# Optimization experiments

Measured on AMD Instinct MI355X. Metric: run time of the kernel, lower is better.

Reference implementation:

```python
import jax, jax.numpy as jnp
import numpy as np

N, H, B = 4096, 128, 32
K_MSG, K_INT = 32, 20
CUTOFFS = (3.0, 3.0, 6.0, 6.0, 10.0, 10.0)  # two EGNN layers per backbone
silu = jax.nn.silu


def _lin(key, fi, fo):
    s = 1.0 / np.sqrt(fi)
    return jax.random.uniform(key, (fi, fo), jnp.float32, -s, s)


def setup_inputs():
    ks = jax.random.split(jax.random.key(0), 16)
    L = 6

    def stack(k, fi, fo):
        return jnp.stack([_lin(kk, fi, fo) for kk in jax.random.split(k, L)])

    return dict(
        h=jax.random.normal(ks[0], (N, H), jnp.float32),
        pos=3.0 * jax.random.normal(ks[1], (N, 3), jnp.float32),
        batch=jnp.sort(jax.random.randint(ks[2], (N,), 0, B)),
        edge_w1=stack(ks[3], 2 * H + 1, H), edge_b1=jnp.zeros((L, H)),
        edge_w2=stack(ks[4], H, H), edge_b2=jnp.zeros((L, H)),
        coord_w1=stack(ks[5], H, H), coord_b1=jnp.zeros((L, H)),
        coord_w2=stack(ks[6], H, 1),
        node_w1=stack(ks[7], 2 * H, H), node_b1=jnp.zeros((L, H)),
        node_w2=stack(ks[8], H, H), node_b2=jnp.zeros((L, H)),
        fw1=_lin(ks[9], H, 128), fb1=jnp.zeros((128,)),
        fw2=_lin(ks[10], 128, 3), fb2=jnp.zeros((3,)),
        iw=jnp.stack([_lin(kk, 2 * H + 2, 1) for kk in jax.random.split(ks[11], 3)]),
        ib=jnp.zeros((3, 1)),
        cw1=_lin(ks[12], H, 128), cb1=jnp.zeros((128,)),
        cw2=_lin(ks[13], 128, 64), cb2=jnp.zeros((64,)),
        sw=_lin(ks[14], H, 1), sb=jnp.zeros((1,)),
    )


def _neighbors(pos, batch, cutoff, k):
    # radius graph with fixed fan-out: k nearest same-graph neighbors within cutoff
    p = jax.lax.stop_gradient(pos)
    d2 = jnp.sum((p[:, None, :] - p[None, :, :]) ** 2, -1)  # [N,N]
    valid = (batch[:, None] == batch[None, :]) & (~jnp.eye(p.shape[0], dtype=bool)) & (d2 <= cutoff * cutoff)
    neg, idx = jax.lax.top_k(jnp.where(valid, -d2, -jnp.inf), k)
    return idx, neg > -jnp.inf  # [N,k] int, [N,k] bool validity mask


def _egnn_layer(h, pos, idx, mask, ew1, eb1, ew2, eb2, cw1, cb1, cw2, nw1, nb1, nw2, nb2):
    mf = mask[..., None].astype(h.dtype)  # [N,K,1]
    hj = h[idx]                            # [N,K,H] gather
    rel = pos[:, None, :] - pos[idx]       # [N,K,3]
    d2 = jnp.sum(rel * rel, -1, keepdims=True)
    hi = jnp.broadcast_to(h[:, None, :], hj.shape)
    m = silu(jnp.concatenate([hi, hj, d2], -1) @ ew1 + eb1)
    m = silu(m @ ew2 + eb2) * mf           # masked messages [N,K,H]
    c = silu(m @ cw1 + cb1) @ cw2          # per-edge coord weight [N,K,1]
    cnt = jnp.maximum(jnp.sum(mf, 1), 1.0)
    pos = pos + jnp.sum(rel * c * mf, 1) / cnt
    h = h + (silu(jnp.concatenate([h, jnp.sum(m, 1)], -1) @ nw1 + nb1) @ nw2 + nb2)
    return h, pos


def _forward(h, pos, batch, edge_w1, edge_b1, edge_w2, edge_b2, coord_w1, coord_b1, coord_w2,
             node_w1, node_b1, node_w2, node_b2, fw1, fb1, fw2, fb2, iw, ib, cw1, cb1, cw2, cb2, sw, sb):
    idx = mask = None
    for l in range(6):  # short(3.0) x2, medium(6.0) x2, long(10.0) x2
        if l % 2 == 0:
            idx, mask = _neighbors(pos, batch, CUTOFFS[l], K_MSG)
        h, pos = _egnn_layer(h, pos, idx, mask, edge_w1[l], edge_b1[l], edge_w2[l], edge_b2[l],
                             coord_w1[l], coord_b1[l], coord_w2[l],
                             node_w1[l], node_b1[l], node_w2[l], node_b2[l])
    forces = jnp.tanh(h @ fw1 + fb1) @ fw2 + fb2
    # interaction detection: radius graph (r=10, max 20 neighbors)
    iidx, imask = _neighbors(pos, batch, 10.0, K_INT)
    rel = pos[:, None, :] - pos[iidx]
    dist = jnp.sqrt(jnp.sum(rel * rel, -1, keepdims=True) + 1e-12)  # [N,K,1]
    hi = jnp.broadcast_to(h[:, None, :], (h.shape[0], K_INT, h.shape[1]))
    feats = jnp.concatenate([hi, h[iidx], dist, dist / 10.0], -1)  # [N,K,2H+2]
    scores = jax.nn.sigmoid(jnp.einsum('nkf,tfo->tnko', feats, iw) + ib[:, None, None, :])
    scores = scores * imask[None, :, :, None].astype(h.dtype)  # zero padded edges
    conformer = jax.nn.relu(h @ cw1 + cb1) @ cw2 + cb2
    steric = h @ sw + sb
    return h, pos, forces, scores[0], scores[1], scores[2], conformer, steric


def reference(h, pos, batch, edge_w1, edge_b1, edge_w2, edge_b2, coord_w1, coord_b1, coord_w2,
              node_w1, node_b1, node_w2, node_b2, fw1, fb1, fw2, fb2, iw, ib, cw1, cb1, cw2, cb2, sw, sb):
    return _forward(h, pos, batch, edge_w1, edge_b1, edge_w2, edge_b2, coord_w1, coord_b1, coord_w2,
                    node_w1, node_b1, node_w2, node_b2, fw1, fb1, fw2, fb2, iw, ib, cw1, cb1, cw2, cb2, sw, sb)
```

## Files before the change

kernel.cpp:

```cpp
#include <hip/hip_runtime.h>
#include <hip/hip_bf16.h>

#define NN 4096
#define HD 128
#define KE 32
#define KI 20
#define XLD 132
#define PLOF 68

#define OFF_H   0
#define OFF_POS 524288
#define OFF_F   536576
#define OFF_S   548864
#define OFF_C   794624
#define OFF_ST  1056768

typedef unsigned short u16;
typedef unsigned int u32;
typedef unsigned long long u64;
typedef __attribute__((ext_vector_type(8))) short bf16x8;
typedef __attribute__((ext_vector_type(4))) float f32x4;

#define PERM_HI 0x07060302u
#define PERM_LO 0x05040100u

__device__ __forceinline__ float b2f(u16 u) {
  union { u32 i; float f; } c; c.i = ((u32)u) << 16; return c.f;
}
__device__ __forceinline__ float silu_f(float x) { return x / (1.f + __expf(-x)); }
__device__ __forceinline__ void stout(void* out, int fp32m, size_t i, float v) {
  if (fp32m) ((float*)out)[i] = v;
  else ((__hip_bfloat16*)out)[i] = __float2bfloat16(v);
}
__device__ __forceinline__ u32 f2b(float f) {
  u32 u = __float_as_uint(f);
  return (u + 0x7fffu + ((u >> 16) & 1u)) >> 16;
}
__device__ __forceinline__ void packhl2(float a, float b, u32& pa, u32& pb) {
  u32 H, L;
  asm("v_cvt_pk_bf16_f32 %0, %1, %2" : "=v"(H) : "v"(a), "v"(b));
  float hfa = __uint_as_float(H << 16);
  float hfb = __uint_as_float(H & 0xffff0000u);
  asm("v_cvt_pk_bf16_f32 %0, %1, %2" : "=v"(L) : "v"(a - hfa), "v"(b - hfb));
  pa = __builtin_amdgcn_perm(H, L, PERM_LO);
  pb = __builtin_amdgcn_perm(H, L, PERM_HI);
}
__device__ __forceinline__ void packplane(float a, float b, u32& H, u32& L) {
  asm("v_cvt_pk_bf16_f32 %0, %1, %2" : "=v"(H) : "v"(a), "v"(b));
  float hfa = __uint_as_float(H << 16);
  float hfb = __uint_as_float(H & 0xffff0000u);
  asm("v_cvt_pk_bf16_f32 %0, %1, %2" : "=v"(L) : "v"(a - hfa), "v"(b - hfb));
}
__device__ __forceinline__ bf16x8 mk8(u32 a, u32 b, u32 c, u32 d) {
  union { u32 u[4]; bf16x8 v; } t;
  t.u[0] = a; t.u[1] = b; t.u[2] = c; t.u[3] = d; return t.v;
}

__global__ void probe_dtype(const u16* __restrict__ h, int* __restrict__ flag) {
  if (threadIdx.x == 0) atomicExch(flag, 0);
  __syncthreads();
  int bad = 0;
  for (int i = threadIdx.x; i < 8192; i += 256) {
    float v = b2f(h[i]);
    if (!(v > -1000.f && v < 1000.f)) bad = 1;
  }
  if (bad) atomicOr(flag, 1);
}

struct CvtTable {
  const void* src[25];
  int dstoff[25];
  int cnt[25];
};

__global__ void convert_all(CvtTable tab, float* __restrict__ wsf, const int* __restrict__ flag) {
  const int seg = blockIdx.y;
  const int i = blockIdx.x * 256 + threadIdx.x;
  if (i >= tab.cnt[seg]) return;
  float v;
  if (*flag) v = ((const float*)tab.src[seg])[i];
  else       v = b2f(((const u16*)tab.src[seg])[i]);
  wsf[tab.dstoff[seg] + i] = v;
}

__global__ void pack_weights(const float* __restrict__ wsf, int offEW1, int offEW2, int offCW1,
                             u16* __restrict__ WBP) {
  int tid = blockIdx.x * 256 + threadIdx.x;
  if (tid >= 18 * 32768) return;
  int m = tid >> 15;
  int rix = tid & 32767;
  int layer = m / 3, s = m % 3;
  const float* src;
  if (s == 0)      src = wsf + offEW1 + (size_t)layer * 257 * HD + 128 * HD;
  else if (s == 1) src = wsf + offEW2 + (size_t)layer * HD * HD;
  else             src = wsf + offCW1 + (size_t)layer * HD * HD;
  int jh = rix & 15, lane = (rix >> 4) & 63, ot = (rix >> 10) & 7, kt = rix >> 13;
  int j = jh & 7;
  int f = kt * 32 + (lane >> 4) * 8 + j;
  int o = ot * 16 + (lane & 15);
  float v = src[f * HD + o];
  u32 hb = f2b(v);
  float hf = __uint_as_float(hb << 16);
  u32 lb = f2b(v - hf);
  WBP[tid] = (jh < 8) ? (u16)hb : (u16)lb;
}

__global__ void graph_bounds(const int* __restrict__ batch, int* __restrict__ gstart) {
  int n = blockIdx.x * 256 + threadIdx.x;
  if (n >= NN) return;
  int v = batch[n];
  int pv = (n == 0) ? -1 : batch[n - 1];
  for (int b = pv + 1; b <= v; b++) gstart[b] = n;
  if (n == NN - 1) for (int b = v + 1; b <= 32; b++) gstart[b] = NN;
}

__global__ __launch_bounds__(256) void neigh_kernel(
    const float* __restrict__ pos, const int* __restrict__ batch,
    const int* __restrict__ gstart, int* __restrict__ idx, int* __restrict__ cnt,
    int Ksel, float cut2) {
  const int lane = threadIdx.x & 63;
  const int i = blockIdx.x * 4 + (threadIdx.x >> 6);
  const int b = batch[i];
  const int gs = gstart[b];
  const int ge = gstart[b + 1];
  const int span = ge - gs;
  const float px = pos[i * 3 + 0], py = pos[i * 3 + 1], pz = pos[i * 3 + 2];
  u64 key[16];
#pragma unroll
  for (int tq = 0; tq < 16; tq++) {
    u64 k64 = ~0ull;
    if (tq * 64 < span) {
      int j = gs + tq * 64 + lane;
      if (j < ge && j != i) {
        float dx = px - pos[j * 3 + 0];
        float dy = py - pos[j * 3 + 1];
        float dz = pz - pos[j * 3 + 2];
        float d2 = dx * dx + dy * dy + dz * dz;
        if (d2 <= cut2) k64 = (((u64)__float_as_uint(d2)) << 32) | (u32)j;
      }
    }
    key[tq] = k64;
  }
  u64 thresh = 0;
  int myidx = i;
  int mycnt = 0;
  for (int s = 0; s < Ksel; s++) {
    u64 m = ~0ull;
#pragma unroll
    for (int tq = 0; tq < 16; tq++) {
      if (tq * 64 < span) {
        u64 kk = key[tq];
        if (kk >= thresh && kk < m) m = kk;
      }
    }
    for (int off = 32; off > 0; off >>= 1) {
      u64 o = __shfl_down(m, (unsigned)off, 64);
      if (o < m) m = o;
    }
    m = __shfl(m, 0, 64);
    if (m != ~0ull) {
      if (lane == s) myidx = (int)(m & 0xffffffffu);
      mycnt++;
      thresh = m + 1;
    } else break;
  }
  if (lane < Ksel) idx[i * Ksel + lane] = myidx;
  if (lane == 0) cnt[i] = mycnt;
}

__device__ __forceinline__ void mfma_stageP(const u32* xp_, const u16* __restrict__ WP,
                                            int w, int lane, f32x4 acc[4]) {
  const int l16 = lane & 15, q = lane >> 4;
  f32x4 z = {0.f, 0.f, 0.f, 0.f};
  acc[0] = z; acc[1] = z; acc[2] = z; acc[3] = z;
#pragma unroll
  for (int kt = 0; kt < 4; kt++) {
    const u16* wb = WP + (size_t)(((kt * 8 + w) * 64 + lane)) * 16;
    bf16x8 wh = *(const bf16x8*)(wb);
    bf16x8 wl = *(const bf16x8*)(wb + 8);
#pragma unroll
    for (int Et = 0; Et < 4; Et++) {
      const u32* xr = xp_ + (Et * 16 + l16) * XLD + kt * 16 + q * 4;
      bf16x8 ah = *(const bf16x8*)(xr);
      bf16x8 al = *(const bf16x8*)(xr + PLOF);
      acc[Et] = __builtin_amdgcn_mfma_f32_16x16x32_bf16(al, wh, acc[Et], 0, 0, 0);
      acc[Et] = __builtin_amdgcn_mfma_f32_16x16x32_bf16(ah, wl, acc[Et], 0, 0, 0);
      acc[Et] = __builtin_amdgcn_mfma_f32_16x16x32_bf16(ah, wh, acc[Et], 0, 0, 0);
    }
  }
}

__device__ __forceinline__ void mfma_stageI(const u32* xp_, const u16* __restrict__ WP,
                                            int w, int lane, f32x4 acc[4]) {
  const int l16 = lane & 15, q = lane >> 4;
  f32x4 z = {0.f, 0.f, 0.f, 0.f};
  acc[0] = z; acc[1] = z; acc[2] = z; acc[3] = z;
#pragma unroll
  for (int kt = 0; kt < 4; kt++) {
    const u16* wb = WP + (size_t)(((kt * 8 + w) * 64 + lane)) * 16;
    bf16x8 wh = *(const bf16x8*)(wb);
    bf16x8 wl = *(const bf16x8*)(wb + 8);
#pragma unroll
    for (int Et = 0; Et < 4; Et++) {
      const u32* xr = xp_ + (Et * 16 + l16) * XLD + kt * 32 + q * 8;
      uint4 xa = *(const uint4*)(xr);
      uint4 xb = *(const uint4*)(xr + 4);
      bf16x8 ah = mk8(__builtin_amdgcn_perm(xa.y, xa.x, PERM_HI),
                      __builtin_amdgcn_perm(xa.w, xa.z, PERM_HI),
                      __builtin_amdgcn_perm(xb.y, xb.x, PERM_HI),
                      __builtin_amdgcn_perm(xb.w, xb.z, PERM_HI));
      bf16x8 al = mk8(__builtin_amdgcn_perm(xa.y, xa.x, PERM_LO),
                      __builtin_amdgcn_perm(xa.w, xa.z, PERM_LO),
                      __builtin_amdgcn_perm(xb.y, xb.x, PERM_LO),
                      __builtin_amdgcn_perm(xb.w, xb.z, PERM_LO));
      acc[Et] = __builtin_amdgcn_mfma_f32_16x16x32_bf16(al, wh, acc[Et], 0, 0, 0);
      acc[Et] = __builtin_amdgcn_mfma_f32_16x16x32_bf16(ah, wl, acc[Et], 0, 0, 0);
      acc[Et] = __builtin_amdgcn_mfma_f32_16x16x32_bf16(ah, wh, acc[Et], 0, 0, 0);
    }
  }
}

__global__ __launch_bounds__(512, 4) void egnn_layer(
    const float* __restrict__ h_in, const float* __restrict__ pos_in,
    float* __restrict__ h_out, float* __restrict__ pos_out,
    const int* __restrict__ idx, const int* __restrict__ cnt,
    const float* __restrict__ ew1, const float* __restrict__ eb1,
    const float* __restrict__ eb2,
    const float* __restrict__ cb1, const float* __restrict__ cw2,
    const float* __restrict__ nw1, const float* __restrict__ nb1,
    const float* __restrict__ nw2, const float* __restrict__ nb2,
    const u16* __restrict__ wbp) {
  __shared__ __align__(16) u32 xp[64 * XLD];
  __shared__ float hi_s[2][HD], hpart_s[2][HD], msum_s[2][HD], u_s[2][HD];
  __shared__ float red_s[512];
  __shared__ float ce_red[64][8];
  __shared__ float rel_s[3][64], d2_s[64], mf_s[64], ce_s[64];
  __shared__ int idx_s[64], cn_s[2];

  const int t = threadIdx.x;
  const int i0 = blockIdx.x * 2;
  const int e = t & 63;
  const int lane = t & 63;
  const int w = __builtin_amdgcn_readfirstlane(t >> 6);
  const int l16 = lane & 15, q = lane >> 4;
  const int o = w * 16 + l16;

  if (t < 64) idx_s[t] = idx[(size_t)(i0 + (t >> 5)) * KE + (t & 31)];
  else if (t < 66) cn_s[t - 64] = cnt[i0 + (t - 64)];
  if (t >= 256) {
    const int nt = t - 256;
    hi_s[nt >> 7][nt & 127] = h_in[(size_t)(i0 + (nt >> 7)) * HD + (nt & 127)];
  }
  __syncthreads();

  if (t < 64) {
    const int nd = t >> 5, ic = i0 + nd;
    const int j = idx_s[t];
    const float rx = pos_in[ic * 3 + 0] - pos_in[j * 3 + 0];
    const float ry = pos_in[ic * 3 + 1] - pos_in[j * 3 + 1];
    const float rz = pos_in[ic * 3 + 2] - pos_in[j * 3 + 2];
    rel_s[0][t] = rx; rel_s[1][t] = ry; rel_s[2][t] = rz;
    d2_s[t] = rx * rx + ry * ry + rz * rz;
    mf_s[t] = ((t & 31) < cn_s[nd]) ? 1.0f : 0.0f;
  }
  {
    const int j = idx_s[e];
    const int f0 = (t >> 6) * 16;
    const float4* src = (const float4*)(h_in + (size_t)j * HD + f0);
    u32* dh = xp + e * XLD + (f0 >> 1);
#pragma unroll
    for (int qq = 0; qq < 4; qq++) {
      float4 v = src[qq];
      u32 H0, L0, H1, L1;
      packplane(v.x, v.y, H0, L0);
      packplane(v.z, v.w, H1, L1);
      uint2 hh; hh.x = H0; hh.y = H1;
      uint2 ll; ll.x = L0; ll.y = L1;
      *(uint2*)(dh + qq * 2) = hh;
      *(uint2*)(dh + PLOF + qq * 2) = ll;
    }
  }
  {
    const int oo = t & 127, nd = (t >> 7) & 1, hf = t >> 8;
    const float* hsrc = hi_s[nd];
    float hp = 0.f;
#pragma unroll
    for (int f4 = hf * 16; f4 < hf * 16 + 16; f4++) {
      float4 xv = *(const float4*)(hsrc + f4 * 4);
      hp = fmaf(xv.x, ew1[(f4 * 4 + 0) * HD + oo], hp);
      hp = fmaf(xv.y, ew1[(f4 * 4 + 1) * HD + oo], hp);
      hp = fmaf(xv.z, ew1[(f4 * 4 + 2) * HD + oo], hp);
      hp = fmaf(xv.w, ew1[(f4 * 4 + 3) * HD + oo], hp);
    }
    red_s[t] = hp;
  }
  __syncthreads();
  if (t < 256) hpart_s[t >> 7][t & 127] = red_s[t] + red_s[t + 256] + eb1[t & 127];
  __syncthreads();

  {
    f32x4 acc[4];
    mfma_stageP(xp, wbp, w, lane, acc);
    __syncthreads();
    const float w2 = ew1[256 * HD + o];
#pragma unroll
    for (int Et = 0; Et < 4; Et++) {
      const float hp = hpart_s[Et >> 1][o];
      const int e0 = Et * 16 + q * 4;
      float s0 = silu_f(acc[Et][0] + hp + d2_s[e0 + 0] * w2);
      float s1 = silu_f(acc[Et][1] + hp + d2_s[e0 + 1] * w2);
      float s2 = silu_f(acc[Et][2] + hp + d2_s[e0 + 2] * w2);
      float s3 = silu_f(acc[Et][3] + hp + d2_s[e0 + 3] * w2);
      u32 p0, p1, p2, p3;
      packhl2(s0, s1, p0, p1);
      packhl2(s2, s3, p2, p3);
      u32* dst = xp + e0 * XLD + o;
      dst[0] = p0; dst[XLD] = p1; dst[2 * XLD] = p2; dst[3 * XLD] = p3;
    }
  }
  __syncthreads();

  {
    f32x4 acc[4];
    mfma_stageI(xp, wbp + 32768, w, lane, acc);
    __syncthreads();
    const float bb = eb2[o];
    float ms0 = 0.f, ms1 = 0.f;
#pragma unroll
    for (int Et = 0; Et < 4; Et++) {
      const int e0 = Et * 16 + q * 4;
      float mm0 = (mf_s[e0 + 0] != 0.f) ? silu_f(acc[Et][0] + bb) : 0.f;
      float mm1 = (mf_s[e0 + 1] != 0.f) ? silu_f(acc[Et][1] + bb) : 0.f;
      float mm2 = (mf_s[e0 + 2] != 0.f) ? silu_f(acc[Et][2] + bb) : 0.f;
      float mm3 = (mf_s[e0 + 3] != 0.f) ? silu_f(acc[Et][3] + bb) : 0.f;
      if (Et < 2) { ms0 += mm0; ms0 += mm1; ms0 += mm2; ms0 += mm3; }
      else        { ms1 += mm0; ms1 += mm1; ms1 += mm2; ms1 += mm3; }
      u32 p0, p1, p2, p3;
      packhl2(mm0, mm1, p0, p1);
      packhl2(mm2, mm3, p2, p3);
      u32* dst = xp + e0 * XLD + o;
      dst[0] = p0; dst[XLD] = p1; dst[2 * XLD] = p2; dst[3 * XLD] = p3;
    }
    ms0 += __shfl_xor(ms0, 16); ms0 += __shfl_xor(ms0, 32);
    ms1 += __shfl_xor(ms1, 16); ms1 += __shfl_xor(ms1, 32);
    if (lane < 16) {
      msum_s[0][w * 16 + lane] = ms0;
      msum_s[1][w * 16 + lane] = ms1;
    }
  }
  __syncthreads();

  {
    f32x4 acc[4];
    mfma_stageI(xp, wbp + 65536, w, lane, acc);
    const float b1 = cb1[o], c2 = cw2[o];
#pragma unroll
    for (int Et = 0; Et < 4; Et++) {
      const int e0 = Et * 16 + q * 4;
#pragma unroll
      for (int r = 0; r < 4; r++) {
        float p = silu_f(acc[Et][r] + b1) * c2;
        p += __shfl_xor(p, 1);
        p += __shfl_xor(p, 2);
        p += __shfl_xor(p, 4);
        p += __shfl_xor(p, 8);
        if (l16 == 0) ce_red[e0 + r][w] = p;
      }
    }
  }
  __syncthreads();
  if (t < 64) {
    float c = 0.f;
#pragma unroll
    for (int wv = 0; wv < 8; wv++) c += ce_red[t][wv];
    ce_s[t] = (mf_s[t] != 0.f) ? c : 0.f;
  }
  __syncthreads();
  if (t < 6) {
    const int nd = t / 3, ax = t - nd * 3, ic = i0 + nd;
    float s = 0.f;
#pragma unroll
    for (int k = 0; k < 32; k++) s = fmaf(rel_s[ax][nd * 32 + k], ce_s[nd * 32 + k], s);
    const float cntf = fmaxf((float)cn_s[nd], 1.f);
    pos_out[ic * 3 + ax] = pos_in[ic * 3 + ax] + s / cntf;
  }
  {
    const int oo = t & 127, nd = (t >> 7) & 1, ph = t >> 8;
    const float* src = ph ? msum_s[nd] : hi_s[nd];
    const float* Wp = nw1 + (size_t)ph * 128 * HD + oo;
    float p = 0.f;
#pragma unroll
    for (int f4 = 0; f4 < 32; f4++) {
      float4 xv = *(const float4*)(src + f4 * 4);
      p = fmaf(xv.x, Wp[(f4 * 4 + 0) * HD], p);
      p = fmaf(xv.y, Wp[(f4 * 4 + 1) * HD], p);
      p = fmaf(xv.z, Wp[(f4 * 4 + 2) * HD], p);
      p = fmaf(xv.w, Wp[(f4 * 4 + 3) * HD], p);
    }
    red_s[t] = p;
  }
  __syncthreads();
  if (t < 256) u_s[t >> 7][t & 127] = silu_f(red_s[t] + red_s[t + 256] + nb1[t & 127]);
  __syncthreads();
  {
    const int oo = t & 127, nd = (t >> 7) & 1, ph = t >> 8;
    const float* src = u_s[nd] + ph * 64;
    const float* Wp = nw2 + (size_t)ph * 64 * HD + oo;
    float p = 0.f;
#pragma unroll
    for (int f4 = 0; f4 < 16; f4++) {
      float4 xv = *(const float4*)(src + f4 * 4);
      p = fmaf(xv.x, Wp[(f4 * 4 + 0) * HD], p);
      p = fmaf(xv.y, Wp[(f4 * 4 + 1) * HD], p);
      p = fmaf(xv.z, Wp[(f4 * 4 + 2) * HD], p);
      p = fmaf(xv.w, Wp[(f4 * 4 + 3) * HD], p);
    }
    red_s[t] = p;
  }
  __syncthreads();
  if (t < 256) {
    const int nd = t >> 7, oo = t & 127;
    h_out[(size_t)(i0 + nd) * HD + oo] = hi_s[nd][oo] + red_s[t] + red_s[t + 256] + nb2[oo];
  }
}

__global__ __launch_bounds__(256) void heads_kernel(
    const float* __restrict__ h, const float* __restrict__ pos,
    const float* __restrict__ fw1, const float* __restrict__ fb1,
    const float* __restrict__ fw2, const float* __restrict__ fb2,
    const float* __restrict__ cw1g, const float* __restrict__ cb1g,
    const float* __restrict__ cw2g, const float* __restrict__ cb2g,
    const float* __restrict__ sw, const float* __restrict__ sb,
    const float* __restrict__ iw,
    float* __restrict__ At, float* __restrict__ Bt,
    void* __restrict__ out, const int* __restrict__ flag) {
  __shared__ float hi_s[HD], v1[HD], red_s[256];
  const int i = blockIdx.x, t = threadIdx.x;
  const int fm = *flag;
  if (t < HD) hi_s[t] = h[(size_t)i * HD + t];
  __syncthreads();
  const int o = t & 127, ph = t >> 7;
  {
    float p = 0.f;
#pragma unroll 4
    for (int f = ph * 64; f < ph * 64 + 64; f++) p = fmaf(hi_s[f], fw1[f * HD + o], p);
    red_s[t] = p;
  }
  __syncthreads();
  if (t < HD) v1[t] = tanhf(red_s[t] + red_s[t + 128] + fb1[t]);
  __syncthreads();
  if (t < 3) {
    float p = 0.f;
    for (int f = 0; f < HD; f++) p = fmaf(v1[f], fw2[f * 3 + t], p);
    stout(out, fm, OFF_F + (size_t)i * 3 + t, p + fb2[t]);
  }
  __syncthreads();
  {
    float p = 0.f;
#pragma unroll 4
    for (int f = ph * 64; f < ph * 64 + 64; f++) p = fmaf(hi_s[f], cw1g[f * HD + o], p);
    red_s[t] = p;
  }
  __syncthreads();
  if (t < HD) v1[t] = fmaxf(red_s[t] + red_s[t + 128] + cb1g[t], 0.f);
  __syncthreads();
  {
    const int oo = t & 63, pc = t >> 6;
    float p = 0.f;
#pragma unroll 4
    for (int f = pc * 32; f < pc * 32 + 32; f++) p = fmaf(v1[f], cw2g[f * 64 + oo], p);
    red_s[t] = p;
  }
  __syncthreads();
  if (t < 64)
    stout(out, fm, OFF_C + (size_t)i * 64 + t,
          red_s[t] + red_s[t + 64] + red_s[t + 128] + red_s[t + 192] + cb2g[t]);
  __syncthreads();
  if (t < HD) red_s[t] = hi_s[t] * sw[t];
  __syncthreads();
  if (t == 0) {
    float p = 0.f;
    for (int f = 0; f < HD; f++) p += red_s[f];
    stout(out, fm, OFF_ST + (size_t)i, p + sb[0]);
  }
  __syncthreads();
  {
    const int g = t >> 5, l = t & 31;
    float p = 0.f;
    if (g < 6) {
      const int tt = g >> 1, half = g & 1;
#pragma unroll
      for (int r2 = 0; r2 < 4; r2++)
        p = fmaf(hi_s[l * 4 + r2], iw[tt * 258 + half * 128 + l * 4 + r2], p);
    }
    red_s[t] = p;
  }
  __syncthreads();
  if (t < 6) {
    float p = 0.f;
    for (int l = 0; l < 32; l++) p += red_s[t * 32 + l];
    const int tt = t >> 1;
    if ((t & 1) == 0) At[tt * NN + i] = p;
    else Bt[tt * NN + i] = p;
  }
  if (t < HD) stout(out, fm, OFF_H + (size_t)i * HD + t, hi_s[t]);
  if (t >= 128 && t < 131) stout(out, fm, OFF_POS + (size_t)i * 3 + (t - 128), pos[i * 3 + (t - 128)]);
}

__global__ void scores_kernel(const float* __restrict__ pos, const int* __restrict__ idx2,
                              const int* __restrict__ cnt2, const float* __restrict__ At,
                              const float* __restrict__ Bt, const float* __restrict__ iw,
                              const float* __restrict__ ib, void* __restrict__ out,
                              const int* __restrict__ flag) {
  int tid = blockIdx.x * 256 + threadIdx.x;
  if (tid >= 3 * NN * KI) return;
  const int fm = *flag;
  const int tt = tid / (NN * KI);
  const int r = tid % (NN * KI);
  const int n = r / KI;
  const int k = r % KI;
  float v = 0.f;
  if (k < cnt2[n]) {
    int j = idx2[n * KI + k];
    float dx = pos[n * 3 + 0] - pos[j * 3 + 0];
    float dy = pos[n * 3 + 1] - pos[j * 3 + 1];
    float dz = pos[n * 3 + 2] - pos[j * 3 + 2];
    float d2 = dx * dx + dy * dy + dz * dz;
    float dist = sqrtf(d2 + 1e-12f);
    float s = At[tt * NN + n] + Bt[tt * NN + j] + dist * iw[tt * 258 + 256] +
              (dist * 0.1f) * iw[tt * 258 + 257] + ib[tt];
    v = 1.f / (1.f + __expf(-s));
  }
  stout(out, fm, OFF_S + (size_t)tid, v);
}

extern "C" void kernel_launch(void* const* d_in, const int* in_sizes, int n_in,
                              void* d_out, int out_size, void* d_ws, size_t ws_size,
                              hipStream_t stream) {
  (void)in_sizes; (void)n_in; (void)out_size; (void)ws_size;

  float* wsf = (float*)d_ws;
  float* h_a = wsf + 0;
  float* pos_a = wsf + 524288;
  float* h_b = wsf + 536576;
  float* pos_b = wsf + 1060864;
  float* At = wsf + 1073152;
  float* Bt = wsf + 1085440;
  const int W0 = 1097728;

  static const int wcnt[23] = {197376, 768, 98304, 768, 98304, 768, 768,
                               196608, 768, 98304, 768, 16384, 128, 384, 3,
                               774, 3, 16384, 128, 8192, 64, 128, 1};
  int woff[23];
  {
    int o = W0;
    for (int k = 0; k < 23; k++) { woff[k] = o; o += wcnt[k]; }
  }
  const int IOFF = woff[22] + wcnt[22];
  int* ibase = (int*)d_ws;
  int* idx1 = ibase + IOFF;
  int* cnt1 = idx1 + NN * KE;
  int* idx2 = cnt1 + NN;
  int* cnt2 = idx2 + NN * KI;
  int* gstart = cnt2 + NN;
  int* flag = gstart + 33;
  int wboff = (int)((flag + 1) - ibase);
  wboff = (wboff + 3) & ~3;
  u16* WBP = (u16*)(ibase + wboff);

  const float* EW1 = wsf + woff[0];
  const float* EB1 = wsf + woff[1];
  const float* EB2 = wsf + woff[3];
  const float* CB1 = wsf + woff[5];
  const float* CW2 = wsf + woff[6];
  const float* NW1 = wsf + woff[7];
  const float* NB1 = wsf + woff[8];
  const float* NW2 = wsf + woff[9];
  const float* NB2 = wsf + woff[10];
  const float* FW1 = wsf + woff[11];
  const float* FB1 = wsf + woff[12];
  const float* FW2 = wsf + woff[13];
  const float* FB2 = wsf + woff[14];
  const float* IW = wsf + woff[15];
  const float* IB = wsf + woff[16];
  const float* CW1G = wsf + woff[17];
  const float* CB1G = wsf + woff[18];
  const float* CW2G = wsf + woff[19];
  const float* CB2G = wsf + woff[20];
  const float* SW = wsf + woff[21];
  const float* SB = wsf + woff[22];

  probe_dtype<<<1, 256, 0, stream>>>((const u16*)d_in[0], flag);

  CvtTable tab;
  tab.src[0] = d_in[0]; tab.dstoff[0] = 0;       tab.cnt[0] = NN * HD;
  tab.src[1] = d_in[1]; tab.dstoff[1] = 524288;  tab.cnt[1] = NN * 3;
  for (int k = 0; k < 23; k++) {
    tab.src[2 + k] = d_in[3 + k];
    tab.dstoff[2 + k] = woff[k];
    tab.cnt[2 + k] = wcnt[k];
  }
  {
    dim3 g((NN * HD + 255) / 256, 25, 1);
    convert_all<<<g, 256, 0, stream>>>(tab, wsf, flag);
  }
  pack_weights<<<(18 * 32768 + 255) / 256, 256, 0, stream>>>(
      wsf, woff[0], woff[2], woff[4], WBP);

  const int* batch = (const int*)d_in[2];
  graph_bounds<<<NN / 256, 256, 0, stream>>>(batch, gstart);

  const float cut2s[3] = {9.f, 36.f, 100.f};
  float *hin = h_a, *pin = pos_a, *hout = h_b, *pout = pos_b;
  for (int l = 0; l < 6; l++) {
    if ((l & 1) == 0)
      neigh_kernel<<<NN / 4, 256, 0, stream>>>(pin, batch, gstart, idx1, cnt1, KE, cut2s[l >> 1]);
    egnn_layer<<<NN / 2, 512, 0, stream>>>(
        hin, pin, hout, pout, idx1, cnt1,
        EW1 + (size_t)l * 257 * HD, EB1 + (size_t)l * HD,
        EB2 + (size_t)l * HD,
        CB1 + (size_t)l * HD, CW2 + (size_t)l * HD,
        NW1 + (size_t)l * 256 * HD, NB1 + (size_t)l * HD,
        NW2 + (size_t)l * HD * HD, NB2 + (size_t)l * HD,
        WBP + (size_t)l * 3 * 32768);
    float* th = hin; hin = hout; hout = th;
    float* tp = pin; pin = pout; pout = tp;
  }
  neigh_kernel<<<NN / 4, 256, 0, stream>>>(pin, batch, gstart, idx2, cnt2, KI, 100.f);
  heads_kernel<<<NN, 256, 0, stream>>>(hin, pin, FW1, FB1, FW2, FB2, CW1G, CB1G, CW2G, CB2G,
                                       SW, SB, IW, At, Bt, d_out, flag);
  scores_kernel<<<(3 * NN * KI + 255) / 256, 256, 0, stream>>>(
      pin, idx2, cnt2, At, Bt, IW, IB, d_out, flag);
}
```

Before: 867.2 us.

## Skip empty edge tiles and transpose MFMA operands to unify plane layout

Counts valid neighbors per node and skips the 16-edge MFMA tiles, gathers and epilogues that hold only padded edges. It swaps the MFMA operand order so outputs are laid out along features. This lets every stage write split hi/lo bf16 planes directly and drops the permute-based stageI path. Reductions are reorganised to match the new output layout. This adds branch divergence risk only at the block level, since the counts are wave-uniform.

```diff
diff --git a/kernel.cpp b/kernel.cpp
--- a/kernel.cpp
+++ b/kernel.cpp
@@ -21,9 +21,6 @@
 typedef __attribute__((ext_vector_type(8))) short bf16x8;
 typedef __attribute__((ext_vector_type(4))) float f32x4;
 
-#define PERM_HI 0x07060302u
-#define PERM_LO 0x05040100u
-
 __device__ __forceinline__ float b2f(u16 u) {
   union { u32 i; float f; } c; c.i = ((u32)u) << 16; return c.f;
 }
@@ -35,25 +32,12 @@
 __device__ __forceinline__ u32 f2b(float f) {
   u32 u = __float_as_uint(f);
   return (u + 0x7fffu + ((u >> 16) & 1u)) >> 16;
-}
-__device__ __forceinline__ void packhl2(float a, float b, u32& pa, u32& pb) {
-  u32 H, L;
-  asm("v_cvt_pk_bf16_f32 %0, %1, %2" : "=v"(H) : "v"(a), "v"(b));
-  float hfa = __uint_as_float(H << 16);
-  float hfb = __uint_as_float(H & 0xffff0000u);
-  asm("v_cvt_pk_bf16_f32 %0, %1, %2" : "=v"(L) : "v"(a - hfa), "v"(b - hfb));
-  pa = __builtin_amdgcn_perm(H, L, PERM_LO);
-  pb = __builtin_amdgcn_perm(H, L, PERM_HI);
 }
 __device__ __forceinline__ void packplane(float a, float b, u32& H, u32& L) {
   asm("v_cvt_pk_bf16_f32 %0, %1, %2" : "=v"(H) : "v"(a), "v"(b));
   float hfa = __uint_as_float(H << 16);
   float hfb = __uint_as_float(H & 0xffff0000u);
   asm("v_cvt_pk_bf16_f32 %0, %1, %2" : "=v"(L) : "v"(a - hfa), "v"(b - hfb));
-}
-__device__ __forceinline__ bf16x8 mk8(u32 a, u32 b, u32 c, u32 d) {
-  union { u32 u[4]; bf16x8 v; } t;
-  t.u[0] = a; t.u[1] = b; t.u[2] = c; t.u[3] = d; return t.v;
 }
 
 __global__ void probe_dtype(const u16* __restrict__ h, int* __restrict__ flag) {
@@ -168,54 +152,27 @@
   if (lane == 0) cnt[i] = mycnt;
 }
 
-__device__ __forceinline__ void mfma_stageP(const u32* xp_, const u16* __restrict__ WP,
-                                            int w, int lane, f32x4 acc[4]) {
+__device__ __forceinline__ void mfma_stageS(const u32* xp_, const u16* __restrict__ WP,
+                                            int w, int lane, int nt0, int nt1,
+                                            f32x4 acc[4]) {
   const int l16 = lane & 15, q = lane >> 4;
   f32x4 z = {0.f, 0.f, 0.f, 0.f};
   acc[0] = z; acc[1] = z; acc[2] = z; acc[3] = z;
 #pragma unroll
   for (int kt = 0; kt < 4; kt++) {
-    const u16* wb = WP + (size_t)(((kt * 8 + w) * 64 + lane)) * 16;
+    const u16* wb = WP + (size_t)((kt * 8 + w) * 64 + lane) * 16;
     bf16x8 wh = *(const bf16x8*)(wb);
     bf16x8 wl = *(const bf16x8*)(wb + 8);
 #pragma unroll
     for (int Et = 0; Et < 4; Et++) {
-      const u32* xr = xp_ + (Et * 16 + l16) * XLD + kt * 16 + q * 4;
-      bf16x8 ah = *(const bf16x8*)(xr);
-      bf16x8 al = *(const bf16x8*)(xr + PLOF);
-      acc[Et] = __builtin_amdgcn_mfma_f32_16x16x32_bf16(al, wh, acc[Et], 0, 0, 0);
-      acc[Et] = __builtin_amdgcn_mfma_f32_16x16x32_bf16(ah, wl, acc[Et], 0, 0, 0);
-      acc[Et] = __builtin_amdgcn_mfma_f32_16x16x32_bf16(ah, wh, acc[Et], 0, 0, 0);
-    }
-  }
-}
-
-__device__ __forceinline__ void mfma_stageI(const u32* xp_, const u16* __restrict__ WP,
-                                            int w, int lane, f32x4 acc[4]) {
-  const int l16 = lane & 15, q = lane >> 4;
-  f32x4 z = {0.f, 0.f, 0.f, 0.f};
-  acc[0] = z; acc[1] = z; acc[2] = z; acc[3] = z;
-#pragma unroll
-  for (int kt = 0; kt < 4; kt++) {
-    const u16* wb = WP + (size_t)(((kt * 8 + w) * 64 + lane)) * 16;
-    bf16x8 wh = *(const bf16x8*)(wb);
-    bf16x8 wl = *(const bf16x8*)(wb + 8);
-#pragma unroll
-    for (int Et = 0; Et < 4; Et++) {
-      const u32* xr = xp_ + (Et * 16 + l16) * XLD + kt * 32 + q * 8;
-      uint4 xa = *(const uint4*)(xr);
-      uint4 xb = *(const uint4*)(xr + 4);
-      bf16x8 ah = mk8(__builtin_amdgcn_perm(xa.y, xa.x, PERM_HI),
-                      __builtin_amdgcn_perm(xa.w, xa.z, PERM_HI),
-                      __builtin_amdgcn_perm(xb.y, xb.x, PERM_HI),
-                      __builtin_amdgcn_perm(xb.w, xb.z, PERM_HI));
-      bf16x8 al = mk8(__builtin_amdgcn_perm(xa.y, xa.x, PERM_LO),
-                      __builtin_amdgcn_perm(xa.w, xa.z, PERM_LO),
-                      __builtin_amdgcn_perm(xb.y, xb.x, PERM_LO),
-                      __builtin_amdgcn_perm(xb.w, xb.z, PERM_LO));
-      acc[Et] = __builtin_amdgcn_mfma_f32_16x16x32_bf16(al, wh, acc[Et], 0, 0, 0);
-      acc[Et] = __builtin_amdgcn_mfma_f32_16x16x32_bf16(ah, wl, acc[Et], 0, 0, 0);
-      acc[Et] = __builtin_amdgcn_mfma_f32_16x16x32_bf16(ah, wh, acc[Et], 0, 0, 0);
+      if ((Et < 2) ? (Et < nt0) : (Et - 2 < nt1)) {
+        const u32* xr = xp_ + (Et * 16 + l16) * XLD + kt * 16 + q * 4;
+        bf16x8 xh = *(const bf16x8*)(xr);
+        bf16x8 xl = *(const bf16x8*)(xr + PLOF);
+        acc[Et] = __builtin_amdgcn_mfma_f32_16x16x32_bf16(wh, xl, acc[Et], 0, 0, 0);
+        acc[Et] = __builtin_amdgcn_mfma_f32_16x16x32_bf16(wl, xh, acc[Et], 0, 0, 0);
+        acc[Et] = __builtin_amdgcn_mfma_f32_16x16x32_bf16(wh, xh, acc[Et], 0, 0, 0);
+      }
     }
   }
 }
@@ -239,11 +196,9 @@
 
   const int t = threadIdx.x;
   const int i0 = blockIdx.x * 2;
-  const int e = t & 63;
   const int lane = t & 63;
   const int w = __builtin_amdgcn_readfirstlane(t >> 6);
   const int l16 = lane & 15, q = lane >> 4;
-  const int o = w * 16 + l16;
 
   if (t < 64) idx_s[t] = idx[(size_t)(i0 + (t >> 5)) * KE + (t & 31)];
   else if (t < 66) cn_s[t - 64] = cnt[i0 + (t - 64)];
@@ -252,6 +207,9 @@
     hi_s[nt >> 7][nt & 127] = h_in[(size_t)(i0 + (nt >> 7)) * HD + (nt & 127)];
   }
   __syncthreads();
+
+  const int nt0 = __builtin_amdgcn_readfirstlane((cn_s[0] + 15) >> 4);
+  const int nt1 = __builtin_amdgcn_readfirstlane((cn_s[1] + 15) >> 4);
 
   if (t < 64) {
     const int nd = t >> 5, ic = i0 + nd;
@@ -264,20 +222,26 @@
     mf_s[t] = ((t & 31) < cn_s[nd]) ? 1.0f : 0.0f;
   }
   {
-    const int j = idx_s[e];
-    const int f0 = (t >> 6) * 16;
-    const float4* src = (const float4*)(h_in + (size_t)j * HD + f0);
-    u32* dh = xp + e * XLD + (f0 >> 1);
-#pragma unroll
-    for (int qq = 0; qq < 4; qq++) {
-      float4 v = src[qq];
-      u32 H0, L0, H1, L1;
-      packplane(v.x, v.y, H0, L0);
-      packplane(v.z, v.w, H1, L1);
-      uint2 hh; hh.x = H0; hh.y = H1;
-      uint2 ll; ll.x = L0; ll.y = L1;
-      *(uint2*)(dh + qq * 2) = hh;
-      *(uint2*)(dh + PLOF + qq * 2) = ll;
+    const int ge_ = t & 63;
+    const int myEt = ge_ >> 4;
+    const bool glive = (myEt < 2) ? (myEt < nt0) : (myEt - 2 < nt1);
+    if (glive) {
+      const int j = idx_s[ge_];
+      const int f0 = (t >> 6) * 16;
+      const float4* src = (const float4*)(h_in + (size_t)j * HD + f0);
+      float4 v0 = src[0], v1 = src[1], v2 = src[2], v3 = src[3];
+      u32 H0, L0, H1, L1, H2, L2, H3, L3, H4, L4, H5, L5, H6, L6, H7, L7;
+      packplane(v0.x, v0.y, H0, L0); packplane(v0.z, v0.w, H1, L1);
+      packplane(v1.x, v1.y, H2, L2); packplane(v1.z, v1.w, H3, L3);
+      packplane(v2.x, v2.y, H4, L4); packplane(v2.z, v2.w, H5, L5);
+      packplane(v3.x, v3.y, H6, L6); packplane(v3.z, v3.w, H7, L7);
+      u32* dh = xp + ge_ * XLD + (f0 >> 1);
+      uint4 a; a.x = H0; a.y = H1; a.z = H2; a.w = H3;
+      uint4 b; b.x = H4; b.y = H5; b.z = H6; b.w = H7;
+      uint4 c; c.x = L0; c.y = L1; c.z = L2; c.w = L3;
+      uint4 d; d.x = L4; d.y = L5; d.z = L6; d.w = L7;
+      *(uint4*)(dh) = a;            *(uint4*)(dh + 4) = b;
+      *(uint4*)(dh + PLOF) = c;     *(uint4*)(dh + PLOF + 4) = d;
     }
   }
   {
@@ -300,71 +264,89 @@
 
   {
     f32x4 acc[4];
-    mfma_stageP(xp, wbp, w, lane, acc);
+    mfma_stageS(xp, wbp, w, lane, nt0, nt1, acc);
     __syncthreads();
-    const float w2 = ew1[256 * HD + o];
+    const float4 w24 = *(const float4*)(ew1 + 256 * HD + w * 16 + q * 4);
 #pragma unroll
     for (int Et = 0; Et < 4; Et++) {
-      const float hp = hpart_s[Et >> 1][o];
-      const int e0 = Et * 16 + q * 4;
-      float s0 = silu_f(acc[Et][0] + hp + d2_s[e0 + 0] * w2);
-      float s1 = silu_f(acc[Et][1] + hp + d2_s[e0 + 1] * w2);
-      float s2 = silu_f(acc[Et][2] + hp + d2_s[e0 + 2] * w2);
-      float s3 = silu_f(acc[Et][3] + hp + d2_s[e0 + 3] * w2);
-      u32 p0, p1, p2, p3;
-      packhl2(s0, s1, p0, p1);
-      packhl2(s2, s3, p2, p3);
-      u32* dst = xp + e0 * XLD + o;
-      dst[0] = p0; dst[XLD] = p1; dst[2 * XLD] = p2; dst[3 * XLD] = p3;
+      if ((Et < 2) ? (Et < nt0) : (Et - 2 < nt1)) {
+        const int ee = Et * 16 + l16;
+        const float d2e = d2_s[ee];
+        const float4 hp4 = *(const float4*)(&hpart_s[Et >> 1][w * 16 + q * 4]);
+        float s0 = silu_f(acc[Et][0] + hp4.x + d2e * w24.x);
+        float s1 = silu_f(acc[Et][1] + hp4.y + d2e * w24.y);
+        float s2 = silu_f(acc[Et][2] + hp4.z + d2e * w24.z);
+        float s3 = silu_f(acc[Et][3] + hp4.w + d2e * w24.w);
+        u32 H0, L0, H1, L1;
+        packplane(s0, s1, H0, L0);
+        packplane(s2, s3, H1, L1);
+        u32* dst = xp + ee * XLD + w * 8 + q * 2;
+        uint2 hh; hh.x = H0; hh.y = H1;
+        uint2 ll; ll.x = L0; ll.y = L1;
+        *(uint2*)(dst) = hh;
+        *(uint2*)(dst + PLOF) = ll;
+      }
     }
   }
   __syncthreads();
 
   {
     f32x4 acc[4];
-    mfma_stageI(xp, wbp + 32768, w, lane, acc);
+    mfma_stageS(xp, wbp + 32768, w, lane, nt0, nt1, acc);
     __syncthreads();
-    const float bb = eb2[o];
-    float ms0 = 0.f, ms1 = 0.f;
+    const float4 eb4 = *(const float4*)(eb2 + w * 16 + q * 4);
+    float ms0x = 0.f, ms0y = 0.f, ms0z = 0.f, ms0w = 0.f;
+    float ms1x = 0.f, ms1y = 0.f, ms1z = 0.f, ms1w = 0.f;
 #pragma unroll
     for (int Et = 0; Et < 4; Et++) {
-      const int e0 = Et * 16 + q * 4;
-      float mm0 = (mf_s[e0 + 0] != 0.f) ? silu_f(acc[Et][0] + bb) : 0.f;
-      float mm1 = (mf_s[e0 + 1] != 0.f) ? silu_f(acc[Et][1] + bb) : 0.f;
-      float mm2 = (mf_s[e0 + 2] != 0.f) ? silu_f(acc[Et][2] + bb) : 0.f;
-      float mm3 = (mf_s[e0 + 3] != 0.f) ? silu_f(acc[Et][3] + bb) : 0.f;
-      if (Et < 2) { ms0 += mm0; ms0 += mm1; ms0 += mm2; ms0 += mm3; }
-      else        { ms1 += mm0; ms1 += mm1; ms1 += mm2; ms1 += mm3; }
-      u32 p0, p1, p2, p3;
-      packhl2(mm0, mm1, p0, p1);
-      packhl2(mm2, mm3, p2, p3);
-      u32* dst = xp + e0 * XLD + o;
-      dst[0] = p0; dst[XLD] = p1; dst[2 * XLD] = p2; dst[3 * XLD] = p3;
-    }
-    ms0 += __shfl_xor(ms0, 16); ms0 += __shfl_xor(ms0, 32);
-    ms1 += __shfl_xor(ms1, 16); ms1 += __shfl_xor(ms1, 32);
-    if (lane < 16) {
-      msum_s[0][w * 16 + lane] = ms0;
-      msum_s[1][w * 16 + lane] = ms1;
+      if ((Et < 2) ? (Et < nt0) : (Et - 2 < nt1)) {
+        const int ee = Et * 16 + l16;
+        const float mfv = mf_s[ee];
+        float m0 = (mfv != 0.f) ? silu_f(acc[Et][0] + eb4.x) : 0.f;
+        float m1 = (mfv != 0.f) ? silu_f(acc[Et][1] + eb4.y) : 0.f;
+        float m2 = (mfv != 0.f) ? silu_f(acc[Et][2] + eb4.z) : 0.f;
+        float m3 = (mfv != 0.f) ? silu_f(acc[Et][3] + eb4.w) : 0.f;
+        if (Et < 2) { ms0x += m0; ms0y += m1; ms0z += m2; ms0w += m3; }
+        else        { ms1x += m0; ms1y += m1; ms1z += m2; ms1w += m3; }
+        u32 H0, L0, H1, L1;
+        packplane(m0, m1, H0, L0);
+        packplane(m2, m3, H1, L1);
+        u32* dst = xp + ee * XLD + w * 8 + q * 2;
+        uint2 hh; hh.x = H0; hh.y = H1;
+        uint2 ll; ll.x = L0; ll.y = L1;
+        *(uint2*)(dst) = hh;
+        *(uint2*)(dst + PLOF) = ll;
+      }
+    }
+#define RED16(v) v += __shfl_xor(v, 1); v += __shfl_xor(v, 2); \
+                 v += __shfl_xor(v, 4); v += __shfl_xor(v, 8);
+    RED16(ms0x) RED16(ms0y) RED16(ms0z) RED16(ms0w)
+    RED16(ms1x) RED16(ms1y) RED16(ms1z) RED16(ms1w)
+#undef RED16
+    if (l16 == 0) {
+      float4 a; a.x = ms0x; a.y = ms0y; a.z = ms0z; a.w = ms0w;
+      float4 b; b.x = ms1x; b.y = ms1y; b.z = ms1z; b.w = ms1w;
+      *(float4*)(&msum_s[0][w * 16 + q * 4]) = a;
+      *(float4*)(&msum_s[1][w * 16 + q * 4]) = b;
     }
   }
   __syncthreads();
 
   {
     f32x4 acc[4];
-    mfma_stageI(xp, wbp + 65536, w, lane, acc);
-    const float b1 = cb1[o], c2 = cw2[o];
+    mfma_stageS(xp, wbp + 65536, w, lane, nt0, nt1, acc);
+    const float4 cb4 = *(const float4*)(cb1 + w * 16 + q * 4);
+    const float4 cw4 = *(const float4*)(cw2 + w * 16 + q * 4);
 #pragma unroll
     for (int Et = 0; Et < 4; Et++) {
-      const int e0 = Et * 16 + q * 4;
-#pragma unroll
-      for (int r = 0; r < 4; r++) {
-        float p = silu_f(acc[Et][r] + b1) * c2;
-        p += __shfl_xor(p, 1);
-        p += __shfl_xor(p, 2);
-        p += __shfl_xor(p, 4);
-        p += __shfl_xor(p, 8);
-        if (l16 == 0) ce_red[e0 + r][w] = p;
+      if ((Et < 2) ? (Et < nt0) : (Et - 2 < nt1)) {
+        float p = silu_f(acc[Et][0] + cb4.x) * cw4.x;
+        p = fmaf(silu_f(acc[Et][1] + cb4.y), cw4.y, p);
+        p = fmaf(silu_f(acc[Et][2] + cb4.z), cw4.z, p);
+        p = fmaf(silu_f(acc[Et][3] + cb4.w), cw4.w, p);
+        p += __shfl_xor(p, 16);
+        p += __shfl_xor(p, 32);
+        if (lane < 16) ce_red[Et * 16 + lane][w] = p;
       }
     }
   }
```

Measured after the change: 860.5 us. Within noise of the previous version (-0.8%).
